# Kernel optimization log

Hardware: AMD Instinct MI355X
Metric: run time of the kernel (lower is better)

## Reference

```python
import jax, jax.numpy as jnp
import numpy as np

N = 50000        # nodes
E = 800000       # edges (before self loops)
F_IN = 64        # num_features
DIM = 64         # num_hidden
C = 10           # num_classes
G = 256          # graphs in batch
NEG_SLOPE = 0.2


def setup_inputs() -> dict:
    key = jax.random.key(0)
    ks = jax.random.split(key, 20)
    def w(k, shape, fan_in):
        return jax.random.normal(k, shape, dtype=jnp.float32) / np.sqrt(fan_in)
    x = jax.random.normal(ks[0], (N, F_IN), dtype=jnp.float32)
    edge_index = jax.random.randint(ks[1], (2, E), 0, N, dtype=jnp.int64)
    batch = jnp.sort(jax.random.randint(ks[2], (N,), 0, G, dtype=jnp.int64))
    return {
        "x": x, "edge_index": edge_index, "batch": batch,
        "w1": w(ks[3], (F_IN, DIM), F_IN), "as1": w(ks[4], (DIM,), DIM), "ad1": w(ks[5], (DIM,), DIM), "b1": jnp.zeros((DIM,), jnp.float32),
        "w2": w(ks[6], (DIM, DIM), DIM),  "as2": w(ks[7], (DIM,), DIM), "ad2": w(ks[8], (DIM,), DIM), "b2": jnp.zeros((DIM,), jnp.float32),
        "w3": w(ks[9], (DIM, DIM), DIM),  "as3": w(ks[10], (DIM,), DIM), "ad3": w(ks[11], (DIM,), DIM), "b3": jnp.zeros((DIM,), jnp.float32),
        "fc1_w": w(ks[12], (DIM, DIM), DIM), "fc1_b": jnp.zeros((DIM,), jnp.float32),
        "fc2_w": w(ks[13], (DIM, C), DIM),   "fc2_b": jnp.zeros((C,), jnp.float32),
    }


def _gat_conv(x, src, dst, w, a_src, a_dst, b, n_nodes):
    # PyG GATConv, heads=1: h = x W; e_ij = LeakyReLU(a_src.h_j + a_dst.h_i);
    # alpha = segment-softmax over edges grouped by target i; out_i = sum_j alpha_ij h_j + b
    h = x @ w                                   # [N, DIM]
    alpha_s = h @ a_src                         # [N]
    alpha_d = h @ a_dst                         # [N]
    e = jax.nn.leaky_relu(alpha_s[src] + alpha_d[dst], NEG_SLOPE)  # [E']
    e_max = jax.ops.segment_max(e, dst, num_segments=n_nodes)
    e_exp = jnp.exp(e - e_max[dst])
    denom = jax.ops.segment_sum(e_exp, dst, num_segments=n_nodes)
    alpha = e_exp / (denom[dst] + 1e-16)        # [E']
    out = jax.ops.segment_sum(alpha[:, None] * h[src], dst, num_segments=n_nodes)
    return out + b


def _l2_normalize(x):
    nrm = jnp.linalg.norm(x, axis=1, keepdims=True)
    return x / jnp.maximum(nrm, 1e-12)


def reference(x, edge_index, batch, w1, as1, ad1, b1, w2, as2, ad2, b2,
              w3, as3, ad3, b3, fc1_w, fc1_b, fc2_w, fc2_b):
    n = x.shape[0]
    loops = jnp.arange(n, dtype=edge_index.dtype)
    src = jnp.concatenate([edge_index[0], loops])   # add_self_loops=True (PyG default)
    dst = jnp.concatenate([edge_index[1], loops])
    h = _gat_conv(x, src, dst, w1, as1, ad1, b1, n)
    h = jax.nn.relu(_l2_normalize(h))
    h = _gat_conv(h, src, dst, w2, as2, ad2, b2, n)
    h = jax.nn.relu(_l2_normalize(h))
    h = _gat_conv(h, src, dst, w3, as3, ad3, b3, n)
    h = jax.nn.relu(_l2_normalize(h))
    g = jax.ops.segment_sum(h, batch, num_segments=G)   # global_add_pool -> [G, DIM]
    g = jax.nn.relu(g @ fc1_w + fc1_b)
    logits = g @ fc2_w + fc2_b
    return jax.nn.log_softmax(logits, axis=-1)
```

## Files before the change

kernel.cpp:

```cpp
#include <hip/hip_runtime.h>
#include <hip/hip_bf16.h>
#include <math.h>

#define DIM 64
#define GNUM 256
#define CNUM 10

__device__ __forceinline__ unsigned bfpack(float a, float b) {
    unsigned ua = __builtin_bit_cast(unsigned, a);
    unsigned ub = __builtin_bit_cast(unsigned, b);
    ua += 0x7fffu + ((ua >> 16) & 1u);
    ub += 0x7fffu + ((ub >> 16) & 1u);
    return (ua >> 16) | (ub & 0xffff0000u);
}
__device__ __forceinline__ float bflo(unsigned u) { return __builtin_bit_cast(float, u << 16); }
__device__ __forceinline__ float bfhi(unsigned u) { return __builtin_bit_cast(float, u & 0xffff0000u); }
__device__ __forceinline__ float bfs(unsigned short u) { return __builtin_bit_cast(float, (unsigned)u << 16); }

__global__ void deg_rank_kernel(const int* __restrict__ ei, int E, int N,
                                int* __restrict__ deg, int* __restrict__ rank) {
    int i = blockIdx.x * blockDim.x + threadIdx.x;
    int EP = E + N;
    if (i >= EP) return;
    int d = (i < E) ? ei[E + i] : (i - E);
    rank[i] = atomicAdd(&deg[d], 1);
}

__global__ __launch_bounds__(256) void scan_misc(const int* __restrict__ deg, int* __restrict__ part, int n, int nb,
                                                 const int* __restrict__ batch, int N,
                                                 int* __restrict__ gstart) {
    int bid = blockIdx.x;
    if (bid < nb) {
        __shared__ int ws[4];
        int i = bid * 256 + threadIdx.x;
        int v = (i < n) ? deg[i] : 0;
        #pragma unroll
        for (int d = 32; d >= 1; d >>= 1) v += __shfl_xor(v, d);
        if ((threadIdx.x & 63) == 0) ws[threadIdx.x >> 6] = v;
        __syncthreads();
        if (threadIdx.x == 0) part[bid] = ws[0] + ws[1] + ws[2] + ws[3];
    } else {
        for (int g = threadIdx.x; g <= GNUM; g += 256) {
            int lo = 0, hi = N;
            while (lo < hi) { int mid = (lo + hi) >> 1; if (batch[mid] < g) lo = mid + 1; else hi = mid; }
            gstart[g] = lo;
        }
    }
}

__global__ __launch_bounds__(256) void scan_down(const int* __restrict__ deg, const int* __restrict__ part,
                                                 int* __restrict__ offs, int n) {
    __shared__ int ws[4];
    __shared__ int base_s;
    int tid = threadIdx.x, lane = tid & 63, wid = tid >> 6;
    int pv = (tid < (int)blockIdx.x) ? part[tid] : 0;
    #pragma unroll
    for (int d = 32; d >= 1; d >>= 1) pv += __shfl_xor(pv, d);
    if (lane == 0) ws[wid] = pv;
    __syncthreads();
    if (tid == 0) base_s = ws[0] + ws[1] + ws[2] + ws[3];
    __syncthreads();
    int i = blockIdx.x * 256 + tid;
    int v = (i < n) ? deg[i] : 0;
    int x = v;
    #pragma unroll
    for (int d = 1; d < 64; d <<= 1) { int t = __shfl_up(x, d); if (lane >= d) x += t; }
    if (lane == 63) ws[wid] = x;
    __syncthreads();
    int add = base_s;
    for (int w = 0; w < wid; ++w) add += ws[w];
    if (i < n) offs[i] = add + x - v;
    if (i == n - 1) offs[n] = add + x;
}

#define XSTR 68
template<bool BF16IN>
__device__ __forceinline__ void mm_tile_body(int bid,
                                             const void* __restrict__ in_, const float* __restrict__ W,
                                             const float* __restrict__ a_s, const float* __restrict__ a_d,
                                             unsigned* __restrict__ hb, float* __restrict__ as_,
                                             float* __restrict__ ad_, int N) {
    __shared__ float Ws[DIM * DIM];
    __shared__ float xT[XSTR * DIM];
    int tid = threadIdx.x;
    int base = bid * 64;

    const float4* W4 = (const float4*)W;
    float4* Ws4 = (float4*)Ws;
    #pragma unroll
    for (int i = 0; i < 4; ++i) Ws4[tid + 256 * i] = W4[tid + 256 * i];

    {
        int row = tid >> 2;
        int kb = (tid & 3) << 4;
        int grow = base + row;
        int crow = grow < N ? grow : N - 1;
        if (BF16IN) {
            const unsigned* xr = (const unsigned*)in_ + ((size_t)crow << 5) + (kb >> 1);
            uint4 u0 = *(const uint4*)xr;
            uint4 u1 = *(const uint4*)(xr + 4);
            xT[(kb + 0) * XSTR + row] = bflo(u0.x);  xT[(kb + 1) * XSTR + row] = bfhi(u0.x);
            xT[(kb + 2) * XSTR + row] = bflo(u0.y);  xT[(kb + 3) * XSTR + row] = bfhi(u0.y);
            xT[(kb + 4) * XSTR + row] = bflo(u0.z);  xT[(kb + 5) * XSTR + row] = bfhi(u0.z);
            xT[(kb + 6) * XSTR + row] = bflo(u0.w);  xT[(kb + 7) * XSTR + row] = bfhi(u0.w);
            xT[(kb + 8) * XSTR + row] = bflo(u1.x);  xT[(kb + 9) * XSTR + row] = bfhi(u1.x);
            xT[(kb + 10) * XSTR + row] = bflo(u1.y); xT[(kb + 11) * XSTR + row] = bfhi(u1.y);
            xT[(kb + 12) * XSTR + row] = bflo(u1.z); xT[(kb + 13) * XSTR + row] = bfhi(u1.z);
            xT[(kb + 14) * XSTR + row] = bflo(u1.w); xT[(kb + 15) * XSTR + row] = bfhi(u1.w);
        } else {
            const float4* xr = (const float4*)((const float*)in_ + ((size_t)crow << 6) + kb);
            float4 v0 = xr[0], v1 = xr[1], v2 = xr[2], v3 = xr[3];
            xT[(kb + 0) * XSTR + row] = v0.x;  xT[(kb + 1) * XSTR + row] = v0.y;
            xT[(kb + 2) * XSTR + row] = v0.z;  xT[(kb + 3) * XSTR + row] = v0.w;
            xT[(kb + 4) * XSTR + row] = v1.x;  xT[(kb + 5) * XSTR + row] = v1.y;
            xT[(kb + 6) * XSTR + row] = v1.z;  xT[(kb + 7) * XSTR + row] = v1.w;
            xT[(kb + 8) * XSTR + row] = v2.x;  xT[(kb + 9) * XSTR + row] = v2.y;
            xT[(kb + 10) * XSTR + row] = v2.z; xT[(kb + 11) * XSTR + row] = v2.w;
            xT[(kb + 12) * XSTR + row] = v3.x; xT[(kb + 13) * XSTR + row] = v3.y;
            xT[(kb + 14) * XSTR + row] = v3.z; xT[(kb + 15) * XSTR + row] = v3.w;
        }
    }
    __syncthreads();

    int tx = tid & 15, ty = tid >> 4;
    int c0 = tx << 2, r0 = ty << 2;
    float acc[4][4] = {{0.f}};
    #pragma unroll 8
    for (int k = 0; k < DIM; ++k) {
        float4 xv = *(const float4*)(xT + k * XSTR + r0);
        float4 wv = *(const float4*)(Ws + k * DIM + c0);
        acc[0][0] += xv.x * wv.x; acc[0][1] += xv.x * wv.y; acc[0][2] += xv.x * wv.z; acc[0][3] += xv.x * wv.w;
        acc[1][0] += xv.y * wv.x; acc[1][1] += xv.y * wv.y; acc[1][2] += xv.y * wv.z; acc[1][3] += xv.y * wv.w;
        acc[2][0] += xv.z * wv.x; acc[2][1] += xv.z * wv.y; acc[2][2] += xv.z * wv.z; acc[2][3] += xv.z * wv.w;
        acc[3][0] += xv.w * wv.x; acc[3][1] += xv.w * wv.y; acc[3][2] += xv.w * wv.z; acc[3][3] += xv.w * wv.w;
    }

    float4 av = *(const float4*)(a_s + c0);
    float4 dv = *(const float4*)(a_d + c0);
    #pragma unroll
    for (int ri = 0; ri < 4; ++ri) {
        int grow = base + r0 + ri;
        float s1 = acc[ri][0] * av.x + acc[ri][1] * av.y + acc[ri][2] * av.z + acc[ri][3] * av.w;
        float s2 = acc[ri][0] * dv.x + acc[ri][1] * dv.y + acc[ri][2] * dv.z + acc[ri][3] * dv.w;
        #pragma unroll
        for (int d = 1; d <= 8; d <<= 1) { s1 += __shfl_xor(s1, d); s2 += __shfl_xor(s2, d); }
        if (grow < N) {
            uint2 o;
            o.x = bfpack(acc[ri][0], acc[ri][1]);
            o.y = bfpack(acc[ri][2], acc[ri][3]);
            *(uint2*)(hb + ((size_t)grow << 5) + (tx << 1)) = o;
            if (tx == 0) { as_[grow] = s1; ad_[grow] = s2; }
        }
    }
}

__global__ __launch_bounds__(256) void mm_tile_bf(const unsigned* __restrict__ in, const float* __restrict__ W,
                                                  const float* __restrict__ a_s, const float* __restrict__ a_d,
                                                  unsigned* __restrict__ hb, float* __restrict__ as_,
                                                  float* __restrict__ ad_, int N) {
    mm_tile_body<true>(blockIdx.x, in, W, a_s, a_d, hb, as_, ad_, N);
}

__global__ __launch_bounds__(256) void mm_fill(const float* __restrict__ in, const float* __restrict__ W,
                                               const float* __restrict__ a_s, const float* __restrict__ a_d,
                                               unsigned* __restrict__ hb, float* __restrict__ as_,
                                               float* __restrict__ ad_, int N, int nbt,
                                               const int* __restrict__ ei, const int* __restrict__ rank, int E,
                                               const int* __restrict__ offs, int2* __restrict__ csr_sd) {
    int bid = blockIdx.x;
    if (bid < nbt) {
        mm_tile_body<false>(bid, in, W, a_s, a_d, hb, as_, ad_, N);
    } else {
        int i = (bid - nbt) * 256 + threadIdx.x;
        int EP = E + N;
        if (i >= EP) return;
        int s, d;
        if (i < E) { s = ei[i]; d = ei[E + i]; } else { s = i - E; d = i - E; }
        csr_sd[offs[d] + rank[i]] = make_int2(s, d);
    }
}

__global__ __launch_bounds__(256) void edge_w(const int2* __restrict__ csr_sd,
                                              const float* __restrict__ as_,
                                              const float* __restrict__ ad_,
                                              int2* __restrict__ ews, int EP) {
    int i = blockIdx.x * 256 + threadIdx.x;
    if (i < 16) ews[EP + i] = make_int2(0, 0);
    if (i >= EP) return;
    int2 sd = csr_sd[i];
    float e = as_[sd.x] + ad_[sd.y];
    e = (e > 0.f) ? e : 0.2f * e;
    float w = expf(e);
    ews[i] = make_int2(sd.x, __builtin_bit_cast(int, w));
}

__global__ __launch_bounds__(256) void gat_agg(const unsigned* __restrict__ hb,
                                               const int2* __restrict__ ews,
                                               const int* __restrict__ offs,
                                               const float* __restrict__ bias,
                                               unsigned* __restrict__ outb, int N) {
    int tid = threadIdx.x, lane = tid & 63, wid = tid >> 6;
    int half = lane >> 5;
    int node = blockIdx.x * 8 + wid * 2 + half;
    int esub = (lane >> 4) & 1, fg = lane & 15;
    int start = 0, deg = 0;
    if (node < N) { start = offs[node]; deg = offs[node + 1] - start; }

    float a0 = 0.f, a1 = 0.f, a2 = 0.f, a3 = 0.f, sw = 0.f;
    for (int i0 = 0; i0 < deg; i0 += 8) {
        int eb = i0 + (esub << 2);
        int t = start + eb;
        int2 eA = ews[t];
        int2 eB = ews[t + 1];
        int2 eC = ews[t + 2];
        int2 eD = ews[t + 3];
        float wA = (eb + 0 < deg) ? __builtin_bit_cast(float, eA.y) : 0.f;
        float wB = (eb + 1 < deg) ? __builtin_bit_cast(float, eB.y) : 0.f;
        float wC = (eb + 2 < deg) ? __builtin_bit_cast(float, eC.y) : 0.f;
        float wD = (eb + 3 < deg) ? __builtin_bit_cast(float, eD.y) : 0.f;
        const uint2 hA = *(const uint2*)(hb + ((size_t)eA.x << 5) + (fg << 1));
        const uint2 hB = *(const uint2*)(hb + ((size_t)eB.x << 5) + (fg << 1));
        const uint2 hC = *(const uint2*)(hb + ((size_t)eC.x << 5) + (fg << 1));
        const uint2 hD = *(const uint2*)(hb + ((size_t)eD.x << 5) + (fg << 1));
        sw += wA + wB + wC + wD;
        a0 += wA * bflo(hA.x) + wB * bflo(hB.x) + wC * bflo(hC.x) + wD * bflo(hD.x);
        a1 += wA * bfhi(hA.x) + wB * bfhi(hB.x) + wC * bfhi(hC.x) + wD * bfhi(hD.x);
        a2 += wA * bflo(hA.y) + wB * bflo(hB.y) + wC * bflo(hC.y) + wD * bflo(hD.y);
        a3 += wA * bfhi(hA.y) + wB * bfhi(hB.y) + wC * bfhi(hC.y) + wD * bfhi(hD.y);
    }
    a0 += __shfl_xor(a0, 16); a1 += __shfl_xor(a1, 16);
    a2 += __shfl_xor(a2, 16); a3 += __shfl_xor(a3, 16);
    sw += __shfl_xor(sw, 16);
    float inv = 1.f / (sw + 1e-16f);
    const float4 bv = *(const float4*)(bias + (fg << 2));
    float o0 = a0 * inv + bv.x, o1 = a1 * inv + bv.y, o2 = a2 * inv + bv.z, o3 = a3 * inv + bv.w;
    float n2 = o0 * o0 + o1 * o1 + o2 * o2 + o3 * o3;
    #pragma unroll
    for (int d = 1; d <= 8; d <<= 1) n2 += __shfl_xor(n2, d);
    float innrm = 1.f / fmaxf(sqrtf(n2), 1e-12f);
    if (esub == 0 && node < N) {
        uint2 o;
        o.x = bfpack(fmaxf(o0 * innrm, 0.f), fmaxf(o1 * innrm, 0.f));
        o.y = bfpack(fmaxf(o2 * innrm, 0.f), fmaxf(o3 * innrm, 0.f));
        *(uint2*)(outb + ((size_t)node << 5) + (fg << 1)) = o;
    }
}

__global__ __launch_bounds__(256) void pool_mlp(const unsigned short* __restrict__ hb, const int* __restrict__ gstart,
                                                const float* __restrict__ fc1w, const float* __restrict__ fc1b,
                                                const float* __restrict__ fc2w, const float* __restrict__ fc2b,
                                                float* __restrict__ out) {
    __shared__ float W1[DIM * DIM];
    __shared__ float red[4 * DIM];
    __shared__ float tbuf[DIM];
    __shared__ float obuf[CNUM];
    int tid = threadIdx.x, lane = tid & 63, wv = tid >> 6;
    int gid = blockIdx.x;

    const float4* W4 = (const float4*)fc1w;
    float4* W1s = (float4*)W1;
    #pragma unroll
    for (int i = 0; i < 4; ++i) W1s[tid + 256 * i] = W4[tid + 256 * i];

    int s = gstart[gid], e = gstart[gid + 1];
    float acc = 0.f;
    for (int i = s + wv; i < e; i += 4) acc += bfs(hb[((size_t)i << 6) + lane]);
    red[wv * DIM + lane] = acc;
    __syncthreads();

    if (wv == 0) {
        float g = red[lane] + red[DIM + lane] + red[2 * DIM + lane] + red[3 * DIM + lane];
        float t = fc1b[lane];
        #pragma unroll
        for (int k = 0; k < DIM; ++k) t += __shfl(g, k) * W1[k * DIM + lane];
        t = fmaxf(t, 0.f);
        tbuf[lane] = t;
        float o = 0.f;
        if (lane < CNUM) {
            o = fc2b[lane];
            #pragma unroll
            for (int k = 0; k < DIM; ++k) o += tbuf[k] * fc2w[k * CNUM + lane];
            obuf[lane] = o;
        }
        if (lane < CNUM) {
            float mx = obuf[0];
            #pragma unroll
            for (int k = 1; k < CNUM; ++k) mx = fmaxf(mx, obuf[k]);
            float ssum = 0.f;
            #pragma unroll
            for (int k = 0; k < CNUM; ++k) ssum += expf(obuf[k] - mx);
            out[gid * CNUM + lane] = o - mx - logf(ssum);
        }
    }
}

static inline size_t align256(size_t x) { return (x + 255) & ~size_t(255); }

extern "C" void kernel_launch(void* const* d_in, const int* in_sizes, int n_in,
                              void* d_out, int out_size, void* d_ws, size_t ws_size,
                              hipStream_t stream) {
    const float* x     = (const float*)d_in[0];
    const int*   ei    = (const int*)d_in[1];
    const int*   batch = (const int*)d_in[2];
    const float* w1  = (const float*)d_in[3];
    const float* as1 = (const float*)d_in[4];
    const float* ad1 = (const float*)d_in[5];
    const float* b1  = (const float*)d_in[6];
    const float* w2  = (const float*)d_in[7];
    const float* as2 = (const float*)d_in[8];
    const float* ad2 = (const float*)d_in[9];
    const float* b2  = (const float*)d_in[10];
    const float* w3  = (const float*)d_in[11];
    const float* as3 = (const float*)d_in[12];
    const float* ad3 = (const float*)d_in[13];
    const float* b3  = (const float*)d_in[14];
    const float* fc1w = (const float*)d_in[15];
    const float* fc1b = (const float*)d_in[16];
    const float* fc2w = (const float*)d_in[17];
    const float* fc2b = (const float*)d_in[18];
    float* out = (float*)d_out;

    int N  = in_sizes[0] / DIM;
    int E  = in_sizes[1] / 2;
    int EP = E + N;
    int nb = (N + 255) / 256;

    char* p = (char*)d_ws;
    unsigned* hbf = (unsigned*)p; p += align256(sizeof(unsigned) * (size_t)N * (DIM / 2));
    unsigned* oAb = (unsigned*)p; p += align256(sizeof(unsigned) * (size_t)N * (DIM / 2));
    unsigned* oBb = (unsigned*)p; p += align256(sizeof(unsigned) * (size_t)N * (DIM / 2));
    float* as_  = (float*)p; p += align256(sizeof(float) * (size_t)N);
    float* ad_  = (float*)p; p += align256(sizeof(float) * (size_t)N);
    int*   deg  = (int*)p;   p += align256(sizeof(int) * (size_t)N);
    int*   offs = (int*)p;   p += align256(sizeof(int) * (size_t)(N + 1));
    int*   rank = (int*)p;   p += align256(sizeof(int) * (size_t)EP);
    int2*  csr_sd = (int2*)p; p += align256(sizeof(int2) * (size_t)EP);
    int2*  ews  = (int2*)p;  p += align256(sizeof(int2) * (size_t)(EP + 16));
    int*   part = (int*)p;   p += align256(sizeof(int) * (size_t)nb);
    int*   gst  = (int*)p;   p += align256(sizeof(int) * (size_t)(GNUM + 1));

    int nblk = (N + 7) / 8;
    int nbt = (N + 63) / 64;
    int epBlocks = (EP + 255) / 256;

    hipMemsetAsync(deg, 0, sizeof(int) * (size_t)N, stream);
    deg_rank_kernel<<<epBlocks, 256, 0, stream>>>(ei, E, N, deg, rank);
    scan_misc<<<nb + 1, 256, 0, stream>>>(deg, part, N, nb, batch, N, gst);
    scan_down<<<nb, 256, 0, stream>>>(deg, part, offs, N);

    mm_fill<<<nbt + epBlocks, 256, 0, stream>>>(x, w1, as1, ad1, hbf, as_, ad_, N, nbt,
                                                ei, rank, E, offs, csr_sd);
    edge_w<<<epBlocks, 256, 0, stream>>>(csr_sd, as_, ad_, ews, EP);
    gat_agg<<<nblk, 256, 0, stream>>>(hbf, ews, offs, b1, oAb, N);
    mm_tile_bf<<<nbt, 256, 0, stream>>>(oAb, w2, as2, ad2, hbf, as_, ad_, N);
    edge_w<<<epBlocks, 256, 0, stream>>>(csr_sd, as_, ad_, ews, EP);
    gat_agg<<<nblk, 256, 0, stream>>>(hbf, ews, offs, b2, oBb, N);
    mm_tile_bf<<<nbt, 256, 0, stream>>>(oBb, w3, as3, ad3, hbf, as_, ad_, N);
    edge_w<<<epBlocks, 256, 0, stream>>>(csr_sd, as_, ad_, ews, EP);
    gat_agg<<<nblk, 256, 0, stream>>>(hbf, ews, offs, b3, oAb, N);

    pool_mlp<<<GNUM, 256, 0, stream>>>((const unsigned short*)oAb, gst, fc1w, fc1b, fc2w, fc2b, out);
}
```

Baseline: 290.5 us.

## Fuse edge-weight computation into GAT aggregation via shared-memory staging

Removes the separate edge_w kernel and its global ews buffer. Each aggregation block now handles 32 nodes, computes the exp attention weights for its contiguous CSR edge range into LDS, then aggregates with 8 lanes per node using 16-byte feature loads. A fallback path recomputes weights from global memory when a block's edge count exceeds the LDS capacity. This cuts a launch and a write-plus-read of the edge array per layer, at the cost of lower parallelism per node and a 16KB LDS footprint per block.

```diff
diff --git a/kernel.cpp b/kernel.cpp
--- a/kernel.cpp
+++ b/kernel.cpp
@@ -180,69 +180,117 @@
     }
 }
 
-__global__ __launch_bounds__(256) void edge_w(const int2* __restrict__ csr_sd,
-                                              const float* __restrict__ as_,
-                                              const float* __restrict__ ad_,
-                                              int2* __restrict__ ews, int EP) {
-    int i = blockIdx.x * 256 + threadIdx.x;
-    if (i < 16) ews[EP + i] = make_int2(0, 0);
-    if (i >= EP) return;
-    int2 sd = csr_sd[i];
-    float e = as_[sd.x] + ad_[sd.y];
-    e = (e > 0.f) ? e : 0.2f * e;
-    float w = expf(e);
-    ews[i] = make_int2(sd.x, __builtin_bit_cast(int, w));
-}
-
+#define AGG_NPB 32
+#define AGG_CAP 2048
 __global__ __launch_bounds__(256) void gat_agg(const unsigned* __restrict__ hb,
-                                               const int2* __restrict__ ews,
+                                               const int2* __restrict__ csr_sd,
+                                               const float* __restrict__ as_,
+                                               const float* __restrict__ ad_,
                                                const int* __restrict__ offs,
                                                const float* __restrict__ bias,
                                                unsigned* __restrict__ outb, int N) {
-    int tid = threadIdx.x, lane = tid & 63, wid = tid >> 6;
-    int half = lane >> 5;
-    int node = blockIdx.x * 8 + wid * 2 + half;
-    int esub = (lane >> 4) & 1, fg = lane & 15;
-    int start = 0, deg = 0;
-    if (node < N) { start = offs[node]; deg = offs[node + 1] - start; }
-
-    float a0 = 0.f, a1 = 0.f, a2 = 0.f, a3 = 0.f, sw = 0.f;
-    for (int i0 = 0; i0 < deg; i0 += 8) {
-        int eb = i0 + (esub << 2);
-        int t = start + eb;
-        int2 eA = ews[t];
-        int2 eB = ews[t + 1];
-        int2 eC = ews[t + 2];
-        int2 eD = ews[t + 3];
-        float wA = (eb + 0 < deg) ? __builtin_bit_cast(float, eA.y) : 0.f;
-        float wB = (eb + 1 < deg) ? __builtin_bit_cast(float, eB.y) : 0.f;
-        float wC = (eb + 2 < deg) ? __builtin_bit_cast(float, eC.y) : 0.f;
-        float wD = (eb + 3 < deg) ? __builtin_bit_cast(float, eD.y) : 0.f;
-        const uint2 hA = *(const uint2*)(hb + ((size_t)eA.x << 5) + (fg << 1));
-        const uint2 hB = *(const uint2*)(hb + ((size_t)eB.x << 5) + (fg << 1));
-        const uint2 hC = *(const uint2*)(hb + ((size_t)eC.x << 5) + (fg << 1));
-        const uint2 hD = *(const uint2*)(hb + ((size_t)eD.x << 5) + (fg << 1));
-        sw += wA + wB + wC + wD;
-        a0 += wA * bflo(hA.x) + wB * bflo(hB.x) + wC * bflo(hC.x) + wD * bflo(hD.x);
-        a1 += wA * bfhi(hA.x) + wB * bfhi(hB.x) + wC * bfhi(hC.x) + wD * bfhi(hD.x);
-        a2 += wA * bflo(hA.y) + wB * bflo(hB.y) + wC * bflo(hC.y) + wD * bflo(hD.y);
-        a3 += wA * bfhi(hA.y) + wB * bfhi(hB.y) + wC * bfhi(hC.y) + wD * bfhi(hD.y);
-    }
-    a0 += __shfl_xor(a0, 16); a1 += __shfl_xor(a1, 16);
-    a2 += __shfl_xor(a2, 16); a3 += __shfl_xor(a3, 16);
-    sw += __shfl_xor(sw, 16);
+    __shared__ int soffs[AGG_NPB + 1];
+    __shared__ float adl[AGG_NPB];
+    __shared__ int2 lsw[AGG_CAP + 4];
+    int tid = threadIdx.x;
+    int base = blockIdx.x * AGG_NPB;
+    if (tid <= AGG_NPB) {
+        int n = base + tid;
+        soffs[tid] = offs[n < N ? n : N];
+    }
+    if (tid < AGG_NPB) {
+        int n = base + tid;
+        adl[tid] = (n < N) ? ad_[n] : 0.f;
+    }
+    __syncthreads();
+    int estart = soffs[0];
+    int nE = soffs[AGG_NPB] - estart;
+    bool inLds = (nE <= AGG_CAP);
+    if (inLds) {
+        for (int i = tid; i < nE; i += 256) {
+            int2 sd = csr_sd[estart + i];
+            float e = as_[sd.x] + adl[sd.y - base];
+            e = (e > 0.f) ? e : 0.2f * e;
+            lsw[i] = make_int2(sd.x, __builtin_bit_cast(int, expf(e)));
+        }
+        if (tid < 4) lsw[nE + tid] = make_int2(0, 0);
+    }
+    __syncthreads();
+
+    int lane = tid & 63, wid = tid >> 6;
+    int sub = lane >> 3, fg = lane & 7;
+    int li = (wid << 3) + sub;
+    int node = base + li;
+    int ls = soffs[li] - estart;
+    int deg = soffs[li + 1] - soffs[li];
+
+    float a0 = 0.f, a1 = 0.f, a2 = 0.f, a3 = 0.f;
+    float a4 = 0.f, a5 = 0.f, a6 = 0.f, a7 = 0.f, sw = 0.f;
+    if (inLds) {
+        for (int eb = 0; eb < deg; eb += 4) {
+            int t = ls + eb;
+            int2 eA = lsw[t], eB = lsw[t + 1], eC = lsw[t + 2], eD = lsw[t + 3];
+            float wA = __builtin_bit_cast(float, eA.y);
+            float wB = (eb + 1 < deg) ? __builtin_bit_cast(float, eB.y) : 0.f;
+            float wC = (eb + 2 < deg) ? __builtin_bit_cast(float, eC.y) : 0.f;
+            float wD = (eb + 3 < deg) ? __builtin_bit_cast(float, eD.y) : 0.f;
+            const uint4 hA = *(const uint4*)(hb + ((size_t)eA.x << 5) + (fg << 2));
+            const uint4 hB = *(const uint4*)(hb + ((size_t)eB.x << 5) + (fg << 2));
+            const uint4 hC = *(const uint4*)(hb + ((size_t)eC.x << 5) + (fg << 2));
+            const uint4 hD = *(const uint4*)(hb + ((size_t)eD.x << 5) + (fg << 2));
+            sw += wA + wB + wC + wD;
+            a0 += wA * bflo(hA.x) + wB * bflo(hB.x) + wC * bflo(hC.x) + wD * bflo(hD.x);
+            a1 += wA * bfhi(hA.x) + wB * bfhi(hB.x) + wC * bfhi(hC.x) + wD * bfhi(hD.x);
+            a2 += wA * bflo(hA.y) + wB * bflo(hB.y) + wC * bflo(hC.y) + wD * bflo(hD.y);
+            a3 += wA * bfhi(hA.y) + wB * bfhi(hB.y) + wC * bfhi(hC.y) + wD * bfhi(hD.y);
+            a4 += wA * bflo(hA.z) + wB * bflo(hB.z) + wC * bflo(hC.z) + wD * bflo(hD.z);
+            a5 += wA * bfhi(hA.z) + wB * bfhi(hB.z) + wC * bfhi(hC.z) + wD * bfhi(hD.z);
+            a6 += wA * bflo(hA.w) + wB * bflo(hB.w) + wC * bflo(hC.w) + wD * bflo(hD.w);
+            a7 += wA * bfhi(hA.w) + wB * bfhi(hB.w) + wC * bfhi(hC.w) + wD * bfhi(hD.w);
+        }
+    } else {
+        float adi = (node < N) ? ad_[node] : 0.f;
+        for (int eb = 0; eb < deg; eb += 4) {
+            int t = estart + ls + eb;
+            float wv[4]; int sv[4];
+            #pragma unroll
+            for (int k = 0; k < 4; ++k) {
+                int tt = t + k;
+                int2 sd = (eb + k < deg) ? csr_sd[tt] : make_int2(0, 0);
+                int s = sd.x; s = s < 0 ? 0 : (s >= N ? N - 1 : s);
+                float e = as_[s] + adi;
+                e = (e > 0.f) ? e : 0.2f * e;
+                wv[k] = (eb + k < deg) ? expf(e) : 0.f;
+                sv[k] = s;
+            }
+            #pragma unroll
+            for (int k = 0; k < 4; ++k) {
+                const uint4 hv = *(const uint4*)(hb + ((size_t)sv[k] << 5) + (fg << 2));
+                sw += wv[k];
+                a0 += wv[k] * bflo(hv.x); a1 += wv[k] * bfhi(hv.x);
+                a2 += wv[k] * bflo(hv.y); a3 += wv[k] * bfhi(hv.y);
+                a4 += wv[k] * bflo(hv.z); a5 += wv[k] * bfhi(hv.z);
+                a6 += wv[k] * bflo(hv.w); a7 += wv[k] * bfhi(hv.w);
+            }
+        }
+    }
+
     float inv = 1.f / (sw + 1e-16f);
-    const float4 bv = *(const float4*)(bias + (fg << 2));
-    float o0 = a0 * inv + bv.x, o1 = a1 * inv + bv.y, o2 = a2 * inv + bv.z, o3 = a3 * inv + bv.w;
-    float n2 = o0 * o0 + o1 * o1 + o2 * o2 + o3 * o3;
-    #pragma unroll
-    for (int d = 1; d <= 8; d <<= 1) n2 += __shfl_xor(n2, d);
+    const float4 b0 = *(const float4*)(bias + (fg << 3));
+    const float4 b1 = *(const float4*)(bias + (fg << 3) + 4);
+    float o0 = a0 * inv + b0.x, o1 = a1 * inv + b0.y, o2 = a2 * inv + b0.z, o3 = a3 * inv + b0.w;
+    float o4 = a4 * inv + b1.x, o5 = a5 * inv + b1.y, o6 = a6 * inv + b1.z, o7 = a7 * inv + b1.w;
+    float n2 = o0 * o0 + o1 * o1 + o2 * o2 + o3 * o3 + o4 * o4 + o5 * o5 + o6 * o6 + o7 * o7;
+    #pragma unroll
+    for (int d = 1; d <= 4; d <<= 1) n2 += __shfl_xor(n2, d);
     float innrm = 1.f / fmaxf(sqrtf(n2), 1e-12f);
-    if (esub == 0 && node < N) {
-        uint2 o;
+    if (node < N) {
+        uint4 o;
         o.x = bfpack(fmaxf(o0 * innrm, 0.f), fmaxf(o1 * innrm, 0.f));
         o.y = bfpack(fmaxf(o2 * innrm, 0.f), fmaxf(o3 * innrm, 0.f));
-        *(uint2*)(outb + ((size_t)node << 5) + (fg << 1)) = o;
+        o.z = bfpack(fmaxf(o4 * innrm, 0.f), fmaxf(o5 * innrm, 0.f));
+        o.w = bfpack(fmaxf(o6 * innrm, 0.f), fmaxf(o7 * innrm, 0.f));
+        *(uint4*)(outb + ((size_t)node << 5) + (fg << 2)) = o;
     }
 }
 
@@ -335,11 +383,10 @@
     int*   offs = (int*)p;   p += align256(sizeof(int) * (size_t)(N + 1));
     int*   rank = (int*)p;   p += align256(sizeof(int) * (size_t)EP);
     int2*  csr_sd = (int2*)p; p += align256(sizeof(int2) * (size_t)EP);
-    int2*  ews  = (int2*)p;  p += align256(sizeof(int2) * (size_t)(EP + 16));
     int*   part = (int*)p;   p += align256(sizeof(int) * (size_t)nb);
     int*   gst  = (int*)p;   p += align256(sizeof(int) * (size_t)(GNUM + 1));
 
-    int nblk = (N + 7) / 8;
+    int nblk = (N + AGG_NPB - 1) / AGG_NPB;
     int nbt = (N + 63) / 64;
     int epBlocks = (EP + 255) / 256;
 
@@ -350,14 +397,11 @@
 
     mm_fill<<<nbt + epBlocks, 256, 0, stream>>>(x, w1, as1, ad1, hbf, as_, ad_, N, nbt,
                                                 ei, rank, E, offs, csr_sd);
-    edge_w<<<epBlocks, 256, 0, stream>>>(csr_sd, as_, ad_, ews, EP);
-    gat_agg<<<nblk, 256, 0, stream>>>(hbf, ews, offs, b1, oAb, N);
+    gat_agg<<<nblk, 256, 0, stream>>>(hbf, csr_sd, as_, ad_, offs, b1, oAb, N);
     mm_tile_bf<<<nbt, 256, 0, stream>>>(oAb, w2, as2, ad2, hbf, as_, ad_, N);
-    edge_w<<<epBlocks, 256, 0, stream>>>(csr_sd, as_, ad_, ews, EP);
-    gat_agg<<<nblk, 256, 0, stream>>>(hbf, ews, offs, b2, oBb, N);
+    gat_agg<<<nblk, 256, 0, stream>>>(hbf, csr_sd, as_, ad_, offs, b2, oBb, N);
     mm_tile_bf<<<nbt, 256, 0, stream>>>(oBb, w3, as3, ad3, hbf, as_, ad_, N);
-    edge_w<<<epBlocks, 256, 0, stream>>>(csr_sd, as_, ad_, ews, EP);
-    gat_agg<<<nblk, 256, 0, stream>>>(hbf, ews, offs, b3, oAb, N);
+    gat_agg<<<nblk, 256, 0, stream>>>(hbf, csr_sd, as_, ad_, offs, b3, oAb, N);
 
     pool_mlp<<<GNUM, 256, 0, stream>>>((const unsigned short*)oAb, gst, fc1w, fc1b, fc2w, fc2b, out);
 }
```

Measured after the change: 266.5 us. 8.3% less time.
